# Kernel optimization log

Measured on AMD Instinct MI355X. Metric: run time of the kernel, lower is better.

Reference implementation:

```python
import jax, jax.numpy as jnp
import numpy as np

D_MODEL = 256
N_HEADS = 8
N_LEVELS = 3
N_POINTS = 4
HEAD_DIM = D_MODEL // N_HEADS
D_FF = 4 * D_MODEL
SHAPES = [(96, 96), (48, 48), (24, 24)]  # (H, W) per level, strides 8/16/32
B = 16
LQ = 64
S = sum(h * w for h, w in SHAPES)  # 12096


def setup_inputs() -> dict:
    key = jax.random.key(0)
    ks = jax.random.split(key, 24)
    rn = lambda k, shp, s=0.02: jax.random.normal(k, shp, jnp.float32) * s
    inp = {}
    inp['text_tokens'] = jax.random.normal(ks[0], (B, LQ, D_MODEL), jnp.float32)
    inp['vis_value'] = jax.random.normal(ks[1], (B, S, D_MODEL), jnp.float32)
    inp['spatial_shapes'] = jnp.array(SHAPES, jnp.int32)
    starts = np.cumsum([0] + [h * w for h, w in SHAPES])[:-1]
    inp['level_start_index'] = jnp.array(starts, jnp.int32)
    inp['vis_key_padding_mask'] = jnp.zeros((B, S), bool)
    # parameters (stored as (in, out))
    inp['ref_w'] = rn(ks[2], (D_MODEL, N_LEVELS * 2));            inp['ref_b'] = jnp.zeros((N_LEVELS * 2,))
    inp['off_w'] = rn(ks[3], (D_MODEL, N_HEADS * N_LEVELS * N_POINTS * 2)); inp['off_b'] = rn(ks[4], (N_HEADS * N_LEVELS * N_POINTS * 2,), 0.5)
    inp['aw_w'] = rn(ks[5], (D_MODEL, N_HEADS * N_LEVELS * N_POINTS));      inp['aw_b'] = jnp.zeros((N_HEADS * N_LEVELS * N_POINTS,))
    inp['val_w'] = rn(ks[6], (D_MODEL, D_MODEL));  inp['val_b'] = jnp.zeros((D_MODEL,))
    inp['proj_w'] = rn(ks[7], (D_MODEL, D_MODEL)); inp['proj_b'] = jnp.zeros((D_MODEL,))
    inp['out_w'] = rn(ks[8], (D_MODEL, D_MODEL));  inp['out_b'] = jnp.zeros((D_MODEL,))
    inp['n1_g'] = jnp.ones((D_MODEL,)); inp['n1_b'] = jnp.zeros((D_MODEL,))
    inp['f1_w'] = rn(ks[9], (D_MODEL, D_FF));  inp['f1_b'] = jnp.zeros((D_FF,))
    inp['f2_w'] = rn(ks[10], (D_FF, D_MODEL)); inp['f2_b'] = jnp.zeros((D_MODEL,))
    inp['n2_g'] = jnp.ones((D_MODEL,)); inp['n2_b'] = jnp.zeros((D_MODEL,))
    return inp


def layer_norm(x, g, b, eps=1e-5):
    m = jnp.mean(x, -1, keepdims=True)
    v = jnp.mean(jnp.square(x - m), -1, keepdims=True)
    return (x - m) * jax.lax.rsqrt(v + eps) * g + b


def ms_deform_sample(value, shapes_np, loc, w):
    """value: (B,S,H,D); loc: (B,Lq,H,L,P,2) in [0,1]; w: (B,Lq,H,L,P) -> (B,Lq,H*D).
    Matches torch grid_sample(bilinear, zero padding, align_corners=False)."""
    Bc, Sc, Hh, Dd = value.shape
    Lq, L, P = loc.shape[1], loc.shape[3], loc.shape[4]
    out = jnp.zeros((Bc, Lq, Hh, Dd), value.dtype)
    start = 0
    for l in range(L):
        Hl, Wl = int(shapes_np[l, 0]), int(shapes_np[l, 1])
        vl = value[:, start:start + Hl * Wl]  # (B, Sl, H, D)
        # reorder sampling coords to (B, Lq*P, H) to align with vl's head axis
        x = (loc[:, :, :, l, :, 0] * Wl - 0.5).transpose(0, 1, 3, 2).reshape(Bc, Lq * P, Hh)
        y = (loc[:, :, :, l, :, 1] * Hl - 0.5).transpose(0, 1, 3, 2).reshape(Bc, Lq * P, Hh)
        x0 = jnp.floor(x); y0 = jnp.floor(y)
        fx = x - x0; fy = y - y0
        ix0 = x0.astype(jnp.int32); iy0 = y0.astype(jnp.int32)
        ix1 = ix0 + 1; iy1 = iy0 + 1

        def gather(ix, iy):
            valid = (ix >= 0) & (ix < Wl) & (iy >= 0) & (iy < Hl)
            idx = jnp.clip(iy, 0, Hl - 1) * Wl + jnp.clip(ix, 0, Wl - 1)
            g = jnp.take_along_axis(vl, idx[..., None], axis=1)  # (B, Lq*P, H, D)
            return g * valid[..., None].astype(value.dtype)

        samp = (gather(ix0, iy0) * ((1 - fx) * (1 - fy))[..., None]
                + gather(ix1, iy0) * (fx * (1 - fy))[..., None]
                + gather(ix0, iy1) * ((1 - fx) * fy)[..., None]
                + gather(ix1, iy1) * (fx * fy)[..., None])
        samp = samp.reshape(Bc, Lq, P, Hh, Dd)
        wl = w[:, :, :, l, :].transpose(0, 1, 3, 2)  # (B, Lq, P, H)
        out = out + jnp.einsum('blphd,blph->blhd', samp, wl)
        start += Hl * Wl
    return out.reshape(Bc, Lq, Hh * Dd)


def reference(text_tokens, vis_value, spatial_shapes, level_start_index, vis_key_padding_mask,
              ref_w, ref_b, off_w, off_b, aw_w, aw_b, val_w, val_b, proj_w, proj_b,
              out_w, out_b, n1_g, n1_b, f1_w, f1_b, f2_w, f2_b, n2_g, n2_b):
    shapes_np = np.asarray(spatial_shapes)  # static level shapes
    Bc, Lq, _ = text_tokens.shape
    Sc = vis_value.shape[1]
    # reference points per level
    ref = jax.nn.sigmoid(text_tokens @ ref_w + ref_b).reshape(Bc, Lq, N_LEVELS, 2)
    # value projection + padding mask
    value = vis_value @ val_w + val_b
    value = jnp.where(vis_key_padding_mask[..., None], 0.0, value)
    value = value.reshape(Bc, Sc, N_HEADS, HEAD_DIM)
    # sampling offsets + attention weights
    off = (text_tokens @ off_w + off_b).reshape(Bc, Lq, N_HEADS, N_LEVELS, N_POINTS, 2)
    aw = (text_tokens @ aw_w + aw_b).reshape(Bc, Lq, N_HEADS, N_LEVELS * N_POINTS)
    aw = jax.nn.softmax(aw, axis=-1).reshape(Bc, Lq, N_HEADS, N_LEVELS, N_POINTS)
    # normalize offsets by (W, H) per level
    normalizer = jnp.stack([jnp.asarray(shapes_np[:, 1], jnp.float32),
                            jnp.asarray(shapes_np[:, 0], jnp.float32)], -1)  # (L, 2)
    loc = ref[:, :, None, :, None, :] + off / normalizer[None, None, None, :, None, :]
    ctx = ms_deform_sample(value, shapes_np, loc, aw)
    ctx = ctx @ proj_w + proj_b  # MSDeformAttn output_proj
    t = layer_norm(text_tokens + (ctx @ out_w + out_b), n1_g, n1_b)
    ffn = jax.nn.relu(t @ f1_w + f1_b) @ f2_w + f2_b
    return layer_norm(t + ffn, n2_g, n2_b)
```

## Files before the change

kernel.cpp:

```cpp
#include <hip/hip_runtime.h>

#define S_TOT 12096
typedef unsigned short u16;
typedef __attribute__((ext_vector_type(4))) unsigned short u16x4;
typedef __attribute__((ext_vector_type(8))) unsigned short u16x8;
typedef __attribute__((ext_vector_type(8))) short bf16x8;
typedef __attribute__((ext_vector_type(4))) float f32x4;

__device__ __forceinline__ u16 f2bf(float f) {
  union { float f; unsigned u; } v; v.f = f;
  unsigned r = v.u + 0x7FFFu + ((v.u >> 16) & 1u);
  return (u16)(r >> 16);
}

__global__ __launch_bounds__(256) void k_pack(
    const float* __restrict__ pw, const float* __restrict__ ow,
    const float* __restrict__ f1w, const float* __restrict__ f2w,
    const float* __restrict__ vw,
    const float* __restrict__ rfw, const float* __restrict__ ofw,
    const float* __restrict__ awW,
    u16* __restrict__ dst) {
  const int t = threadIdx.x;
  const int bid = blockIdx.x;
  if (bid >= 44) {
    int t2 = (bid - 44) * 256 + t;
    int ln = t2 & 63;
    int kc = (t2 >> 6) & 7;
    int nt = t2 >> 9;
    int col = nt * 16 + (ln & 15);
    int k0 = kc * 32 + (ln >> 4) * 8;
    u16x8 v;
#pragma unroll
    for (int e = 0; e < 8; ++e) {
      int k = k0 + e;
      float val;
      if (col < 6)        val = rfw[k * 6 + col];
      else if (col < 198) val = ofw[k * 192 + (col - 6)];
      else if (col < 294) val = awW[k * 96 + (col - 198)];
      else                val = 0.f;
      v[e] = f2bf(val);
    }
    *reinterpret_cast<u16x8*>(dst + ((size_t)81920 + (size_t)(nt * 8 + kc) * 64 + ln) * 8) = v;
    return;
  }
  __shared__ float ls[16384];
  const float* src; int nc, KC, base8, r0;
  if (bid < 4)       { src = pw;  nc = 256;  KC = 8;  base8 = 0;     r0 = bid * 64; }
  else if (bid < 8)  { src = ow;  nc = 256;  KC = 8;  base8 = 8192;  r0 = (bid - 4) * 64; }
  else if (bid < 24) { src = f2w; nc = 256;  KC = 32; base8 = 49152; r0 = (bid - 8) * 64; }
  else if (bid < 40) { src = f1w; nc = 1024; KC = 8;  base8 = 16384; r0 = (bid - 24) * 16; }
  else               { src = vw;  nc = 256;  KC = 8;  base8 = 91648; r0 = (bid - 40) * 64; }
  const float* sp = src + (size_t)r0 * nc;
#pragma unroll
  for (int i = 0; i < 16; ++i) {
    int fi = (i * 256 + t) * 4;
    *reinterpret_cast<float4*>(&ls[fi]) = *reinterpret_cast<const float4*>(sp + fi);
  }
  __syncthreads();
  if (nc == 256) {
    int kc0 = r0 >> 5;
#pragma unroll
    for (int f = 0; f < 8; ++f) {
      int fid = f * 256 + t;
      int kcl = fid >> 10, nt = (fid >> 6) & 15, ln = fid & 63;
      int n = nt * 16 + (ln & 15);
      int rb = kcl * 32 + (ln >> 4) * 8;
      u16x8 v;
#pragma unroll
      for (int e = 0; e < 8; ++e) v[e] = f2bf(ls[(rb + e) * 256 + n]);
      *reinterpret_cast<u16x8*>(
          dst + ((size_t)base8 + (size_t)(nt * KC + kc0 + kcl) * 64 + ln) * 8) = v;
    }
  } else {
    int kc = r0 >> 5, half = (r0 & 16) ? 32 : 0;
#pragma unroll
    for (int f = 0; f < 8; ++f) {
      int fid = f * 256 + t;
      int nt = fid >> 5, lnh = fid & 31;
      int ln = lnh + half;
      int n = nt * 16 + (ln & 15);
      int rb = ((ln >> 4) & 1) * 8;
      u16x8 v;
#pragma unroll
      for (int e = 0; e < 8; ++e) v[e] = f2bf(ls[(rb + e) * 1024 + n]);
      *reinterpret_cast<u16x8*>(
          dst + ((size_t)base8 + (size_t)(nt * 8 + kc) * 64 + ln) * 8) = v;
    }
  }
}

__device__ __forceinline__ int swz(int row, int bytecol, int rowbytes) {
  return (row * rowbytes + bytecol) ^ ((row & 7) << 4);
}

__global__ __launch_bounds__(1024) void k_proj(
    const float* __restrict__ text, const u16* __restrict__ pkp,
    const float* __restrict__ ref_b, const float* __restrict__ off_b,
    const float* __restrict__ aw_b, float* __restrict__ P) {
  __shared__ u16 aT[16 * 256];
  const int tid = threadIdx.x;
  const int lane = tid & 63, wv = tid >> 6;
  const int l15 = lane & 15, lg = lane >> 4;
  const size_t r0 = (size_t)blockIdx.x * 16;
  const f32x4 z4 = {0.f, 0.f, 0.f, 0.f};
  {
    int row = wv, c0 = lane * 4;
    const float* src = text + (r0 + row) * 256 + c0;
    u16x4 v;
#pragma unroll
    for (int j = 0; j < 4; ++j) v[j] = f2bf(src[j]);
    *reinterpret_cast<u16x4*>(reinterpret_cast<char*>(aT) + swz(row, c0 * 2, 512)) = v;
  }
  __syncthreads();
  const int nrep = (wv < 3) ? 2 : 1;
  for (int rep = 0; rep < nrep; ++rep) {
    int nt = wv + rep * 16;
    f32x4 acc = z4;
#pragma unroll
    for (int half = 0; half < 2; ++half) {
      bf16x8 b4[4];
#pragma unroll
      for (int i = 0; i < 4; ++i)
        b4[i] = *reinterpret_cast<const bf16x8*>(pkp + ((size_t)(nt * 8 + half * 4 + i) * 64 + lane) * 8);
#pragma unroll
      for (int i = 0; i < 4; ++i) {
        int kc = half * 4 + i;
        bf16x8 a = *reinterpret_cast<const bf16x8*>(
            reinterpret_cast<const char*>(aT) + swz(l15, kc * 64 + lg * 16, 512));
        acc = __builtin_amdgcn_mfma_f32_16x16x32_bf16(a, b4[i], acc, 0, 0, 0);
      }
    }
    int col = nt * 16 + l15;
    float bias = (col < 6) ? ref_b[col]
               : (col < 198) ? off_b[col - 6]
               : (col < 294) ? aw_b[col - 198] : 0.f;
#pragma unroll
    for (int r = 0; r < 4; ++r) {
      int m = lg * 4 + r;
      P[(r0 + m) * 304 + col] = acc[r] + bias;
    }
  }
}

__global__ __launch_bounds__(256) void k2_fused(
    const float* __restrict__ P, const float* __restrict__ vis,
    const unsigned char* __restrict__ mask,
    float* __restrict__ AGG, float* __restrict__ CSUM) {
  __shared__ float p_s[304];
  __shared__ float ref_s[6];
  __shared__ float aw_s[96];
  const int tid = threadIdx.x;
  const int xcd = blockIdx.x & 7;
  const int idx = blockIdx.x >> 3;
  const int b = xcd * 2 + (idx >> 7);
  const int rem = idx & 127;
  const int bq = b * 64 + (rem >> 1);
  const int hf = rem & 1;
  p_s[tid] = P[(size_t)bq * 304 + tid];
  if (tid < 48) p_s[256 + tid] = P[(size_t)bq * 304 + 256 + tid];
  __syncthreads();
  if (tid < 6) ref_s[tid] = 1.f / (1.f + expf(-p_s[tid]));
  if (tid >= 8 && tid < 16) {
    int hh = tid - 8;
    float mx = -3.4e38f;
    for (int j = 0; j < 12; ++j) mx = fmaxf(mx, p_s[198 + hh * 12 + j]);
    float e[12]; float s = 0.f;
    for (int j = 0; j < 12; ++j) { e[j] = expf(p_s[198 + hh * 12 + j] - mx); s += e[j]; }
    float inv = 1.f / s;
    for (int j = 0; j < 12; ++j) aw_s[hh * 12 + j] = e[j] * inv;
  }
  __syncthreads();

  const int h = tid >> 5, d = tid & 31;
  float agg[8] = {0.f, 0.f, 0.f, 0.f, 0.f, 0.f, 0.f, 0.f};
  float csum = 0.f;
  const unsigned char* maskb = mask + (size_t)b * S_TOT;
  const float* visb = vis + (size_t)b * S_TOT * 256 + d * 8;

  auto do_point = [&](int l, int p, int Wl, int st) {
    const float Wf = (float)Wl;
    const int ip = (h * 3 + l) * 4 + p;
    const float rx = ref_s[l * 2 + 0], ry = ref_s[l * 2 + 1];
    const float ox = p_s[6 + ip * 2 + 0], oy = p_s[6 + ip * 2 + 1];
    const float aww = aw_s[ip];
    const float x = (rx + ox / Wf) * Wf - 0.5f;
    const float y = (ry + oy / Wf) * Wf - 0.5f;
    const float x0f = floorf(x), y0f = floorf(y);
    const float fx = x - x0f, fy = y - y0f;
    const int ix0 = (int)x0f, iy0 = (int)y0f;
    const bool xv0 = (unsigned)ix0 < (unsigned)Wl;
    const bool xv1 = (unsigned)(ix0 + 1) < (unsigned)Wl;
    const bool yv0 = (unsigned)iy0 < (unsigned)Wl;
    const bool yv1 = (unsigned)(iy0 + 1) < (unsigned)Wl;
    const int cx0 = min(max(ix0, 0), Wl - 1), cx1 = min(max(ix0 + 1, 0), Wl - 1);
    const int cy0 = min(max(iy0, 0), Wl - 1), cy1 = min(max(iy0 + 1, 0), Wl - 1);
    const int s00 = st + cy0 * Wl + cx0, s10 = st + cy0 * Wl + cx1;
    const int s01 = st + cy1 * Wl + cx0, s11 = st + cy1 * Wl + cx1;
    float w00 = (yv0 && xv0 && !maskb[s00]) ? aww * (1.f - fx) * (1.f - fy) : 0.f;
    float w10 = (yv0 && xv1 && !maskb[s10]) ? aww * fx * (1.f - fy) : 0.f;
    float w01 = (yv1 && xv0 && !maskb[s01]) ? aww * (1.f - fx) * fy : 0.f;
    float w11 = (yv1 && xv1 && !maskb[s11]) ? aww * fx * fy : 0.f;
    csum += w00 + w10 + w01 + w11;
    const float* p00 = visb + (size_t)s00 * 256;
    const float* p10 = visb + (size_t)s10 * 256;
    const float* p01 = visb + (size_t)s01 * 256;
    const float* p11 = visb + (size_t)s11 * 256;
    float4 a0 = *reinterpret_cast<const float4*>(p00);
    float4 a1 = *reinterpret_cast<const float4*>(p00 + 4);
    float4 b0 = *reinterpret_cast<const float4*>(p10);
    float4 b1 = *reinterpret_cast<const float4*>(p10 + 4);
    float4 c0 = *reinterpret_cast<const float4*>(p01);
    float4 c1 = *reinterpret_cast<const float4*>(p01 + 4);
    float4 e0 = *reinterpret_cast<const float4*>(p11);
    float4 e1 = *reinterpret_cast<const float4*>(p11 + 4);
    agg[0] += w00 * a0.x + w10 * b0.x + w01 * c0.x + w11 * e0.x;
    agg[1] += w00 * a0.y + w10 * b0.y + w01 * c0.y + w11 * e0.y;
    agg[2] += w00 * a0.z + w10 * b0.z + w01 * c0.z + w11 * e0.z;
    agg[3] += w00 * a0.w + w10 * b0.w + w01 * c0.w + w11 * e0.w;
    agg[4] += w00 * a1.x + w10 * b1.x + w01 * c1.x + w11 * e1.x;
    agg[5] += w00 * a1.y + w10 * b1.y + w01 * c1.y + w11 * e1.y;
    agg[6] += w00 * a1.z + w10 * b1.z + w01 * c1.z + w11 * e1.z;
    agg[7] += w00 * a1.w + w10 * b1.w + w01 * c1.w + w11 * e1.w;
  };

  if (hf == 0) {
    do_point(0, 0, 96, 0);
    do_point(0, 1, 96, 0);
    do_point(0, 2, 96, 0);
    do_point(0, 3, 96, 0);
    do_point(1, 0, 48, 9216);
    do_point(1, 1, 48, 9216);
  } else {
    do_point(1, 2, 48, 9216);
    do_point(1, 3, 48, 9216);
    do_point(2, 0, 24, 11520);
    do_point(2, 1, 24, 11520);
    do_point(2, 2, 24, 11520);
    do_point(2, 3, 24, 11520);
  }
  float* ap = AGG + (((size_t)hf * 1024 + bq) * 8 + h) * 256 + d * 8;
  float4 v0 = {agg[0], agg[1], agg[2], agg[3]};
  float4 v1 = {agg[4], agg[5], agg[6], agg[7]};
  *reinterpret_cast<float4*>(ap) = v0;
  *reinterpret_cast<float4*>(ap + 4) = v1;
  if (d == 0) CSUM[((size_t)hf * 1024 + bq) * 8 + h] = csum;
}

__global__ __launch_bounds__(1024) void k_ctx(
    const float* __restrict__ AGG, const float* __restrict__ CSUM,
    const u16* __restrict__ pkv, const float* __restrict__ val_b,
    float* __restrict__ ctx) {
  __shared__ u16 aG[16 * 2048];
  __shared__ float cs_s[16][8];
  const int tid = threadIdx.x;
  const int lane = tid & 63, wv = tid >> 6;
  const int l15 = lane & 15, lg = lane >> 4;
  const size_t r0 = (size_t)blockIdx.x * 16;
  const f32x4 z4 = {0.f, 0.f, 0.f, 0.f};
  {
    int row = tid >> 6, c0 = (tid & 63) * 32;
    const float* s0 = AGG + ((size_t)(r0 + row)) * 2048 + c0;
    const float* s1 = s0 + (size_t)1024 * 2048;
#pragma unroll
    for (int j = 0; j < 4; ++j) {
      float4 x0 = *reinterpret_cast<const float4*>(s0 + j * 8);
      float4 x1 = *reinterpret_cast<const float4*>(s0 + j * 8 + 4);
      float4 y0 = *reinterpret_cast<const float4*>(s1 + j * 8);
      float4 y1 = *reinterpret_cast<const float4*>(s1 + j * 8 + 4);
      u16x8 v;
      v[0] = f2bf(x0.x + y0.x); v[1] = f2bf(x0.y + y0.y);
      v[2] = f2bf(x0.z + y0.z); v[3] = f2bf(x0.w + y0.w);
      v[4] = f2bf(x1.x + y1.x); v[5] = f2bf(x1.y + y1.y);
      v[6] = f2bf(x1.z + y1.z); v[7] = f2bf(x1.w + y1.w);
      *reinterpret_cast<u16x8*>(reinterpret_cast<char*>(aG) +
                                swz(row, (c0 + j * 8) * 2, 4096)) = v;
    }
    if (tid < 128) {
      int rr = tid >> 3, hh = tid & 7;
      cs_s[rr][hh] = CSUM[(r0 + rr) * 8 + hh] + CSUM[(1024 + r0 + rr) * 8 + hh];
    }
  }
  __syncthreads();
  {
    const int h = wv >> 1;
    bf16x8 b8[8];
#pragma unroll
    for (int kc = 0; kc < 8; ++kc)
      b8[kc] = *reinterpret_cast<const bf16x8*>(pkv + ((size_t)(wv * 8 + kc) * 64 + lane) * 8);
    f32x4 acc = z4;
#pragma unroll
    for (int kc = 0; kc < 8; ++kc) {
      bf16x8 a = *reinterpret_cast<const bf16x8*>(
          reinterpret_cast<const char*>(aG) + swz(l15, h * 512 + kc * 64 + lg * 16, 4096));
      acc = __builtin_amdgcn_mfma_f32_16x16x32_bf16(a, b8[kc], acc, 0, 0, 0);
    }
    int col = wv * 16 + l15;
    float vb = val_b[col];
#pragma unroll
    for (int r = 0; r < 4; ++r) {
      int m = lg * 4 + r;
      ctx[(r0 + m) * 256 + col] = acc[r] + cs_s[m][h] * vb;
    }
  }
}

__global__ __launch_bounds__(1024) void k3_mfma(
    const float* __restrict__ ctx, const float* __restrict__ text,
    const u16* __restrict__ pk,
    const float* __restrict__ proj_b, const float* __restrict__ out_b,
    const float* __restrict__ n1_g, const float* __restrict__ n1_b,
    const float* __restrict__ f1_b, const float* __restrict__ f2_b,
    const float* __restrict__ n2_g, const float* __restrict__ n2_b,
    float* __restrict__ outp) {
  __shared__ u16 aA[16 * 256];
  __shared__ u16 aY[16 * 256];
  __shared__ u16 aH[16 * 1024];
  __shared__ float fb[16 * 256];

  const int tid = threadIdx.x;
  const int lane = tid & 63, wv = tid >> 6;
  const int l15 = lane & 15, lg = lane >> 4;
  const size_t r0 = (size_t)blockIdx.x * 16;
  const f32x4 z4 = {0.f, 0.f, 0.f, 0.f};

  {
    int row = wv, c0 = lane * 4;
    const float* src = ctx + (r0 + row) * 256 + c0;
    u16x4 v;
#pragma unroll
    for (int j = 0; j < 4; ++j) v[j] = f2bf(src[j]);
    *reinterpret_cast<u16x4*>(reinterpret_cast<char*>(aA) + swz(row, c0 * 2, 512)) = v;
  }
  __syncthreads();

  {
    f32x4 acc = z4;
#pragma unroll
    for (int half = 0; half < 2; ++half) {
      bf16x8 b4[4];
#pragma unroll
      for (int i = 0; i < 4; ++i)
        b4[i] = *reinterpret_cast<const bf16x8*>(pk + ((wv * 8 + half * 4 + i) * 64 + lane) * 8);
#pragma unroll
      for (int i = 0; i < 4; ++i) {
        int kc = half * 4 + i;
        bf16x8 a = *reinterpret_cast<const bf16x8*>(
            reinterpret_cast<const char*>(aA) + swz(l15, kc * 64 + lg * 16, 512));
        acc = __builtin_amdgcn_mfma_f32_16x16x32_bf16(a, b4[i], acc, 0, 0, 0);
      }
    }
    int col = wv * 16 + l15;
    float bias = proj_b[col];
#pragma unroll
    for (int r = 0; r < 4; ++r) {
      int m = lg * 4 + r;
      *reinterpret_cast<u16*>(reinterpret_cast<char*>(aY) + swz(m, col * 2, 512)) =
          f2bf(acc[r] + bias);
    }
  }
  __syncthreads();

  {
    const u16* pko = pk + 65536;
    f32x4 acc = z4;
#pragma unroll
    for (int half = 0; half < 2; ++half) {
      bf16x8 b4[4];
#pragma unroll
      for (int i = 0; i < 4; ++i)
        b4[i] = *reinterpret_cast<const bf16x8*>(pko + ((wv * 8 + half * 4 + i) * 64 + lane) * 8);
#pragma unroll
      for (int i = 0; i < 4; ++i) {
        int kc = half * 4 + i;
        bf16x8 a = *reinterpret_cast<const bf16x8*>(
            reinterpret_cast<const char*>(aY) + swz(l15, kc * 64 + lg * 16, 512));
        acc = __builtin_amdgcn_mfma_f32_16x16x32_bf16(a, b4[i], acc, 0, 0, 0);
      }
    }
    int col = wv * 16 + l15;
    float bias = out_b[col];
#pragma unroll
    for (int r = 0; r < 4; ++r) {
      int m = lg * 4 + r;
      fb[m * 256 + col] = acc[r] + bias + text[(r0 + m) * 256 + col];
    }
  }
  __syncthreads();

  {
    int row = wv;
    float s = 0.f;
#pragma unroll
    for (int j = 0; j < 4; ++j) s += fb[row * 256 + lane + j * 64];
#pragma unroll
    for (int o = 1; o < 64; o <<= 1) s += __shfl_xor(s, o, 64);
    float mu = s * 0.00390625f;
    float vs = 0.f;
#pragma unroll
    for (int j = 0; j < 4; ++j) {
      float dd = fb[row * 256 + lane + j * 64] - mu; vs += dd * dd;
    }
#pragma unroll
    for (int o = 1; o < 64; o <<= 1) vs += __shfl_xor(vs, o, 64);
    float rs = rsqrtf(vs * 0.00390625f + 1e-5f);
#pragma unroll
    for (int j = 0; j < 4; ++j) {
      int col = lane + j * 64;
      float v = (fb[row * 256 + col] - mu) * rs * n1_g[col] + n1_b[col];
      fb[row * 256 + col] = v;
      *reinterpret_cast<u16*>(reinterpret_cast<char*>(aA) + swz(row, col * 2, 512)) = f2bf(v);
    }
  }
  __syncthreads();

  {
    const u16* pkf1 = pk + 131072;
#pragma unroll
    for (int nt = 0; nt < 4; ++nt) {
      int ntg = wv * 4 + nt;
      f32x4 acc = z4;
#pragma unroll
      for (int half = 0; half < 2; ++half) {
        bf16x8 b4[4];
#pragma unroll
        for (int i = 0; i < 4; ++i)
          b4[i] = *reinterpret_cast<const bf16x8*>(pkf1 + ((ntg * 8 + half * 4 + i) * 64 + lane) * 8);
#pragma unroll
        for (int i = 0; i < 4; ++i) {
          int kc = half * 4 + i;
          bf16x8 a = *reinterpret_cast<const bf16x8*>(
              reinterpret_cast<const char*>(aA) + swz(l15, kc * 64 + lg * 16, 512));
          acc = __builtin_amdgcn_mfma_f32_16x16x32_bf16(a, b4[i], acc, 0, 0, 0);
        }
      }
      int col = ntg * 16 + l15;
      float bias = f1_b[col];
#pragma unroll
      for (int r = 0; r < 4; ++r) {
        int m = lg * 4 + r;
        *reinterpret_cast<u16*>(reinterpret_cast<char*>(aH) + swz(m, col * 2, 2048)) =
            f2bf(fmaxf(acc[r] + bias, 0.f));
      }
    }
  }
  __syncthreads();

  {
    const u16* pkf2 = pk + 393216;
    f32x4 acc = z4;
#pragma unroll
    for (int c = 0; c < 8; ++c) {
      bf16x8 b4[4];
#pragma unroll
      for (int i = 0; i < 4; ++i)
        b4[i] = *reinterpret_cast<const bf16x8*>(pkf2 + ((wv * 32 + c * 4 + i) * 64 + lane) * 8);
#pragma unroll
      for (int i = 0; i < 4; ++i) {
        int kc = c * 4 + i;
        bf16x8 a = *reinterpret_cast<const bf16x8*>(
            reinterpret_cast<const char*>(aH) + swz(l15, kc * 64 + lg * 16, 2048));
        acc = __builtin_amdgcn_mfma_f32_16x16x32_bf16(a, b4[i], acc, 0, 0, 0);
      }
    }
    int col = wv * 16 + l15;
    float bias = f2_b[col];
#pragma unroll
    for (int r = 0; r < 4; ++r) {
      int m = lg * 4 + r;
      fb[m * 256 + col] = acc[r] + bias + fb[m * 256 + col];
    }
  }
  __syncthreads();

  {
    int row = wv;
    float s = 0.f;
#pragma unroll
    for (int j = 0; j < 4; ++j) s += fb[row * 256 + lane + j * 64];
#pragma unroll
    for (int o = 1; o < 64; o <<= 1) s += __shfl_xor(s, o, 64);
    float mu = s * 0.00390625f;
    float vs = 0.f;
#pragma unroll
    for (int j = 0; j < 4; ++j) {
      float dd = fb[row * 256 + lane + j * 64] - mu; vs += dd * dd;
    }
#pragma unroll
    for (int o = 1; o < 64; o <<= 1) vs += __shfl_xor(vs, o, 64);
    float rs = rsqrtf(vs * 0.00390625f + 1e-5f);
#pragma unroll
    for (int j = 0; j < 4; ++j) {
      int col = lane + j * 64;
      outp[(r0 + row) * 256 + col] = (fb[row * 256 + col] - mu) * rs * n2_g[col] + n2_b[col];
    }
  }
}

extern "C" void kernel_launch(void* const* d_in, const int* in_sizes, int n_in,
                              void* d_out, int out_size, void* d_ws, size_t ws_size,
                              hipStream_t stream) {
  const float* text  = (const float*)d_in[0];
  const float* vis   = (const float*)d_in[1];
  const unsigned char* mask = (const unsigned char*)d_in[4];
  const float* ref_w = (const float*)d_in[5];
  const float* ref_b = (const float*)d_in[6];
  const float* off_w = (const float*)d_in[7];
  const float* off_b = (const float*)d_in[8];
  const float* aw_w  = (const float*)d_in[9];
  const float* aw_b  = (const float*)d_in[10];
  const float* val_w = (const float*)d_in[11];
  const float* val_b = (const float*)d_in[12];
  const float* proj_w = (const float*)d_in[13];
  const float* proj_b = (const float*)d_in[14];
  const float* out_w = (const float*)d_in[15];
  const float* out_b = (const float*)d_in[16];
  const float* n1_g  = (const float*)d_in[17];
  const float* n1_b  = (const float*)d_in[18];
  const float* f1_w  = (const float*)d_in[19];
  const float* f1_b  = (const float*)d_in[20];
  const float* f2_w  = (const float*)d_in[21];
  const float* f2_b  = (const float*)d_in[22];
  const float* n2_g  = (const float*)d_in[23];
  const float* n2_b  = (const float*)d_in[24];
  float* outp = (float*)d_out;

  char* ws = (char*)d_ws;
  float* ctx = (float*)ws;
  u16* pk    = (u16*)(ws + (size_t)1024 * 1024);
  u16* pkp   = pk + (size_t)81920 * 8;
  u16* pkv   = pk + (size_t)91648 * 8;
  float* P   = (float*)(ws + (size_t)4 * 1024 * 1024);
  float* AGG = (float*)(ws + (size_t)6 * 1024 * 1024);
  float* CSUM = (float*)(ws + (size_t)23 * 1024 * 1024);

  k_pack<<<82, 256, 0, stream>>>(proj_w, out_w, f1_w, f2_w, val_w,
                                 ref_w, off_w, aw_w, pk);
  k_proj<<<64, 1024, 0, stream>>>(text, pkp, ref_b, off_b, aw_b, P);
  k2_fused<<<2048, 256, 0, stream>>>(P, vis, mask, AGG, CSUM);
  k_ctx<<<64, 1024, 0, stream>>>(AGG, CSUM, pkv, val_b, ctx);
  k3_mfma<<<64, 1024, 0, stream>>>(ctx, text, pk, proj_b, out_b,
                                   n1_g, n1_b, f1_b, f2_b, n2_g, n2_b, outp);
}
```

Measured before the change: 77.43 us.

## Fuse ctx value-projection into final MLP kernel and store AGG as bf16

Merges the k_ctx kernel into k3_mfma, so the value-projection result stays in registers and is written straight to LDS as bf16 instead of round-tripping through a global ctx buffer. The separate kernel launch goes away, and the LDS arrays are aliased into one 64KB buffer. The k2_fused partial aggregates are now stored as bf16 rather than fp32, halving the AGG write and read traffic. The cost is an extra rounding of the two half-sums before they are added, which slightly reduces accuracy.

```diff
diff --git a/kernel.cpp b/kernel.cpp
--- a/kernel.cpp
+++ b/kernel.cpp
@@ -11,6 +11,9 @@
   union { float f; unsigned u; } v; v.f = f;
   unsigned r = v.u + 0x7FFFu + ((v.u >> 16) & 1u);
   return (u16)(r >> 16);
+}
+__device__ __forceinline__ float bf2f(u16 h) {
+  union { unsigned u; float f; } v; v.u = ((unsigned)h) << 16; return v.f;
 }
 
 __global__ __launch_bounds__(256) void k_pack(
@@ -145,7 +148,7 @@
 __global__ __launch_bounds__(256) void k2_fused(
     const float* __restrict__ P, const float* __restrict__ vis,
     const unsigned char* __restrict__ mask,
-    float* __restrict__ AGG, float* __restrict__ CSUM) {
+    u16* __restrict__ AGG, float* __restrict__ CSUM) {
   __shared__ float p_s[304];
   __shared__ float ref_s[6];
   __shared__ float aw_s[96];
@@ -238,40 +241,47 @@
     do_point(2, 2, 24, 11520);
     do_point(2, 3, 24, 11520);
   }
-  float* ap = AGG + (((size_t)hf * 1024 + bq) * 8 + h) * 256 + d * 8;
-  float4 v0 = {agg[0], agg[1], agg[2], agg[3]};
-  float4 v1 = {agg[4], agg[5], agg[6], agg[7]};
-  *reinterpret_cast<float4*>(ap) = v0;
-  *reinterpret_cast<float4*>(ap + 4) = v1;
+  u16x8 v;
+#pragma unroll
+  for (int j = 0; j < 8; ++j) v[j] = f2bf(agg[j]);
+  *reinterpret_cast<u16x8*>(AGG + (((size_t)hf * 1024 + bq) * 8 + h) * 256 + d * 8) = v;
   if (d == 0) CSUM[((size_t)hf * 1024 + bq) * 8 + h] = csum;
 }
 
-__global__ __launch_bounds__(1024) void k_ctx(
-    const float* __restrict__ AGG, const float* __restrict__ CSUM,
-    const u16* __restrict__ pkv, const float* __restrict__ val_b,
-    float* __restrict__ ctx) {
-  __shared__ u16 aG[16 * 2048];
+__global__ __launch_bounds__(1024) void k3_mfma(
+    const u16* __restrict__ AGG, const float* __restrict__ CSUM,
+    const float* __restrict__ text, const u16* __restrict__ pk,
+    const float* __restrict__ val_b,
+    const float* __restrict__ proj_b, const float* __restrict__ out_b,
+    const float* __restrict__ n1_g, const float* __restrict__ n1_b,
+    const float* __restrict__ f1_b, const float* __restrict__ f2_b,
+    const float* __restrict__ n2_g, const float* __restrict__ n2_b,
+    float* __restrict__ outp) {
+  __shared__ char lds[65536];
+  u16* aG = (u16*)lds;
+  u16* aA = (u16*)lds;
+  u16* aY = (u16*)(lds + 8192);
+  u16* aH = (u16*)(lds + 16384);
+  float* fb = (float*)(lds + 49152);
   __shared__ float cs_s[16][8];
+
   const int tid = threadIdx.x;
   const int lane = tid & 63, wv = tid >> 6;
   const int l15 = lane & 15, lg = lane >> 4;
   const size_t r0 = (size_t)blockIdx.x * 16;
   const f32x4 z4 = {0.f, 0.f, 0.f, 0.f};
+
   {
     int row = tid >> 6, c0 = (tid & 63) * 32;
-    const float* s0 = AGG + ((size_t)(r0 + row)) * 2048 + c0;
-    const float* s1 = s0 + (size_t)1024 * 2048;
+    const u16* s0 = AGG + ((size_t)(r0 + row)) * 2048 + c0;
+    const u16* s1 = s0 + (size_t)1024 * 2048;
 #pragma unroll
     for (int j = 0; j < 4; ++j) {
-      float4 x0 = *reinterpret_cast<const float4*>(s0 + j * 8);
-      float4 x1 = *reinterpret_cast<const float4*>(s0 + j * 8 + 4);
-      float4 y0 = *reinterpret_cast<const float4*>(s1 + j * 8);
-      float4 y1 = *reinterpret_cast<const float4*>(s1 + j * 8 + 4);
+      u16x8 x = *reinterpret_cast<const u16x8*>(s0 + j * 8);
+      u16x8 y = *reinterpret_cast<const u16x8*>(s1 + j * 8);
       u16x8 v;
-      v[0] = f2bf(x0.x + y0.x); v[1] = f2bf(x0.y + y0.y);
-      v[2] = f2bf(x0.z + y0.z); v[3] = f2bf(x0.w + y0.w);
-      v[4] = f2bf(x1.x + y1.x); v[5] = f2bf(x1.y + y1.y);
-      v[6] = f2bf(x1.z + y1.z); v[7] = f2bf(x1.w + y1.w);
+#pragma unroll
+      for (int e = 0; e < 8; ++e) v[e] = f2bf(bf2f(x[e]) + bf2f(y[e]));
       *reinterpret_cast<u16x8*>(reinterpret_cast<char*>(aG) +
                                 swz(row, (c0 + j * 8) * 2, 4096)) = v;
     }
@@ -281,7 +291,9 @@
     }
   }
   __syncthreads();
-  {
+  f32x4 ctxacc;
+  {
+    const u16* pkv = pk + (size_t)91648 * 8;
     const int h = wv >> 1;
     bf16x8 b8[8];
 #pragma unroll
@@ -297,39 +309,17 @@
     int col = wv * 16 + l15;
     float vb = val_b[col];
 #pragma unroll
+    for (int r = 0; r < 4; ++r) ctxacc[r] = acc[r] + cs_s[lg * 4 + r][h] * vb;
+  }
+  __syncthreads();
+  {
+    int col = wv * 16 + l15;
+#pragma unroll
     for (int r = 0; r < 4; ++r) {
       int m = lg * 4 + r;
-      ctx[(r0 + m) * 256 + col] = acc[r] + cs_s[m][h] * vb;
-    }
-  }
-}
-
-__global__ __launch_bounds__(1024) void k3_mfma(
-    const float* __restrict__ ctx, const float* __restrict__ text,
-    const u16* __restrict__ pk,
-    const float* __restrict__ proj_b, const float* __restrict__ out_b,
-    const float* __restrict__ n1_g, const float* __restrict__ n1_b,
-    const float* __restrict__ f1_b, const float* __restrict__ f2_b,
-    const float* __restrict__ n2_g, const float* __restrict__ n2_b,
-    float* __restrict__ outp) {
-  __shared__ u16 aA[16 * 256];
-  __shared__ u16 aY[16 * 256];
-  __shared__ u16 aH[16 * 1024];
-  __shared__ float fb[16 * 256];
-
-  const int tid = threadIdx.x;
-  const int lane = tid & 63, wv = tid >> 6;
-  const int l15 = lane & 15, lg = lane >> 4;
-  const size_t r0 = (size_t)blockIdx.x * 16;
-  const f32x4 z4 = {0.f, 0.f, 0.f, 0.f};
-
-  {
-    int row = wv, c0 = lane * 4;
-    const float* src = ctx + (r0 + row) * 256 + c0;
-    u16x4 v;
-#pragma unroll
-    for (int j = 0; j < 4; ++j) v[j] = f2bf(src[j]);
-    *reinterpret_cast<u16x4*>(reinterpret_cast<char*>(aA) + swz(row, c0 * 2, 512)) = v;
+      *reinterpret_cast<u16*>(reinterpret_cast<char*>(aA) + swz(m, col * 2, 512)) =
+          f2bf(ctxacc[r]);
+    }
   }
   __syncthreads();
 
@@ -525,19 +515,16 @@
   float* outp = (float*)d_out;
 
   char* ws = (char*)d_ws;
-  float* ctx = (float*)ws;
-  u16* pk    = (u16*)(ws + (size_t)1024 * 1024);
+  u16* pk    = (u16*)ws;
   u16* pkp   = pk + (size_t)81920 * 8;
-  u16* pkv   = pk + (size_t)91648 * 8;
-  float* P   = (float*)(ws + (size_t)4 * 1024 * 1024);
-  float* AGG = (float*)(ws + (size_t)6 * 1024 * 1024);
-  float* CSUM = (float*)(ws + (size_t)23 * 1024 * 1024);
+  float* P   = (float*)(ws + (size_t)2 * 1024 * 1024);
+  u16* AGG   = (u16*)(ws + (size_t)4 * 1024 * 1024);
+  float* CSUM = (float*)(ws + (size_t)13 * 1024 * 1024);
 
   k_pack<<<82, 256, 0, stream>>>(proj_w, out_w, f1_w, f2_w, val_w,
                                  ref_w, off_w, aw_w, pk);
   k_proj<<<64, 1024, 0, stream>>>(text, pkp, ref_b, off_b, aw_b, P);
   k2_fused<<<2048, 256, 0, stream>>>(P, vis, mask, AGG, CSUM);
-  k_ctx<<<64, 1024, 0, stream>>>(AGG, CSUM, pkv, val_b, ctx);
-  k3_mfma<<<64, 1024, 0, stream>>>(ctx, text, pk, proj_b, out_b,
+  k3_mfma<<<64, 1024, 0, stream>>>(AGG, CSUM, text, pk, val_b, proj_b, out_b,
                                    n1_g, n1_b, f1_b, f2_b, n2_g, n2_b, outp);
 }
```

Result: faster. 66.96 us (-13.5%).
